# Performance work log

Measured on AMD Instinct MI355X. Metric: run time of the kernel, lower is better.

The kernel has to match this reference:

```python
import jax, jax.numpy as jnp
import numpy as np

B, S, D_IN, D_OUT, H = 4, 2048, 1024, 1024, 16
DH = D_OUT // H


def setup_inputs() -> dict:
    key = jax.random.key(0)
    k1, k2, k3 = jax.random.split(key, 3)
    payload = jax.random.normal(k1, (B, S, D_IN), dtype=jnp.float32)
    w_qkv = jax.random.normal(k2, (D_IN, 3 * D_OUT), dtype=jnp.float32) * (D_IN ** -0.5)
    w_out = jax.random.normal(k3, (D_OUT, D_OUT), dtype=jnp.float32) * (D_OUT ** -0.5)
    b_out = jnp.zeros((D_OUT,), dtype=jnp.float32)
    return {"payload": payload, "w_qkv": w_qkv, "w_out": w_out, "b_out": b_out}


def reference(payload, w_qkv, w_out, b_out):
    b, t, _ = payload.shape
    h, dh = H, DH
    qkv = payload @ w_qkv  # [b, t, 3*D_OUT]
    q, k, v = jnp.split(qkv, 3, axis=-1)
    # [b, t, h, dh] -> [b, h, t, dh]
    q = q.reshape(b, t, h, dh).transpose(0, 2, 1, 3)
    k = k.reshape(b, t, h, dh).transpose(0, 2, 1, 3)
    v = v.reshape(b, t, h, dh).transpose(0, 2, 1, 3)
    scores = jnp.einsum("bhqd,bhkd->bhqk", q, k) / jnp.sqrt(jnp.float32(dh))
    causal = jnp.tril(jnp.ones((t, t), dtype=bool))  # True = keep
    scores = jnp.where(causal, scores, -jnp.inf)
    weights = jax.nn.softmax(scores, axis=-1)
    # dropout_rate = 0.0 -> identity
    ctx = jnp.einsum("bhqk,bhkd->bhqd", weights, v)
    ctx = ctx.transpose(0, 2, 1, 3).reshape(b, t, h * dh)
    return ctx @ w_out + b_out
```

## Files before the change

kernel.cpp:

```cpp
#include <hip/hip_runtime.h>

#define NB 4
#define NS 2048
#define NH 16
#define NDH 64

typedef short bf16x8 __attribute__((ext_vector_type(8)));
typedef short bf16x4 __attribute__((ext_vector_type(4)));
typedef float f32x4 __attribute__((ext_vector_type(4)));
typedef unsigned short u16;
typedef unsigned int u32;

static __device__ __forceinline__ u16 f2bf(float f) {
  unsigned u = __float_as_uint(f);
  u += 0x7fffu + ((u >> 16) & 1u);
  return (u16)(u >> 16);
}

#define GLDS(gp, lp) __builtin_amdgcn_global_load_lds( \
    (const __attribute__((address_space(1))) void*)(gp), \
    (__attribute__((address_space(3))) void*)(lp), 16, 0, 0)

__global__ void prep_k(const float* __restrict__ payload, const float* __restrict__ w_qkv,
                       const float* __restrict__ w_out, u16* __restrict__ Xb,
                       u16* __restrict__ Wqkvt, u16* __restrict__ Woutt) {
  __shared__ float t[32][33];
  const int bid = blockIdx.x;
  if (bid < 4096) {
    int i = (bid * 256 + threadIdx.x) * 8;
    float4 a = *(const float4*)&payload[i];
    float4 b = *(const float4*)&payload[i + 4];
    bf16x8 u;
    u[0] = (short)f2bf(a.x); u[1] = (short)f2bf(a.y);
    u[2] = (short)f2bf(a.z); u[3] = (short)f2bf(a.w);
    u[4] = (short)f2bf(b.x); u[5] = (short)f2bf(b.y);
    u[6] = (short)f2bf(b.z); u[7] = (short)f2bf(b.w);
    *(bf16x8*)&Xb[i] = u;
    return;
  }
  const float* in;  u16* out;  int R, C, c0, r0;
  if (bid < 4096 + 3072) {
    int b2 = bid - 4096;
    in = w_qkv; out = Wqkvt; R = 1024; C = 3072;
    c0 = (b2 % 96) * 32; r0 = (b2 / 96) * 32;
  } else {
    int b3 = bid - 7168;
    in = w_out; out = Woutt; R = 1024; C = 1024;
    c0 = (b3 & 31) * 32; r0 = (b3 >> 5) * 32;
  }
  int tx = threadIdx.x & 7, ty = threadIdx.x >> 3;
  float4 v = *(const float4*)&in[(size_t)(r0 + ty) * C + c0 + tx * 4];
  t[ty][tx * 4 + 0] = v.x; t[ty][tx * 4 + 1] = v.y;
  t[ty][tx * 4 + 2] = v.z; t[ty][tx * 4 + 3] = v.w;
  __syncthreads();
  ushort4 o;
  o.x = f2bf(t[tx * 4 + 0][ty]); o.y = f2bf(t[tx * 4 + 1][ty]);
  o.z = f2bf(t[tx * 4 + 2][ty]); o.w = f2bf(t[tx * 4 + 3][ty]);
  *(ushort4*)&out[(size_t)(c0 + ty) * R + r0 + tx * 4] = o;
}

template<int MODE, int WM>
__global__ __launch_bounds__(WM * 128)
void gemm_k(const u16* __restrict__ A, const u16* __restrict__ Bt,
            int M, int N, int K,
            u16* __restrict__ Qo, u16* __restrict__ Ko, u16* __restrict__ VTo,
            float* __restrict__ Co, const float* __restrict__ bias) {
  constexpr int T  = WM * 128;
  constexpr int BM = WM * 64;
  constexpr int RA = 4;
  constexpr int RB = 1024 / T;
  __shared__ __align__(16) u16 As[BM * 64];
  __shared__ __align__(16) u16 Bs[128 * 64];
  const int tid = threadIdx.x;
  const int w = tid >> 6, l = tid & 63;
  const int lr = l & 15, lg = l >> 4;
  const int wr = w >> 1, wc = w & 1;

  const int L = blockIdx.x + gridDim.x * blockIdx.y;
  const int xcd = L & 7, li = L >> 3;
  const int bx = li % gridDim.x;
  const int by = xcd * (gridDim.y >> 3) + li / gridDim.x;

  const int m0 = by * BM, n0 = bx * 128;
  const int swz = (lr & 7) << 4;

  f32x4 acc[4][4] = {};

  const int nk = K >> 6;
  for (int kt = 0; kt < nk; ++kt) {
    __syncthreads();
    const int k0 = kt * 64;
#pragma unroll
    for (int r2 = 0; r2 < RA; ++r2) {
      int c = r2 * T + tid;
      int row = c >> 3;
      int scolb = ((c & 7) * 16) ^ ((row & 7) << 4);
      GLDS(A + (size_t)(m0 + row) * K + k0 + (scolb >> 1),
           (char*)As + (size_t)r2 * T * 16 + w * 1024);
    }
#pragma unroll
    for (int r2 = 0; r2 < RB; ++r2) {
      int c = r2 * T + tid;
      int row = c >> 3;
      int scolb = ((c & 7) * 16) ^ ((row & 7) << 4);
      GLDS(Bt + (size_t)(n0 + row) * K + k0 + (scolb >> 1),
           (char*)Bs + (size_t)r2 * T * 16 + w * 1024);
    }
    __syncthreads();

#pragma unroll
    for (int kk = 0; kk < 2; ++kk) {
      bf16x8 af[4];
#pragma unroll
      for (int mi = 0; mi < 4; ++mi)
        af[mi] = *(const bf16x8*)((const char*)As +
                  ((wr * 64 + mi * 16 + lr) * 128 + ((kk * 64 + lg * 16) ^ swz)));
#pragma unroll
      for (int ni = 0; ni < 4; ++ni) {
        bf16x8 bfr = *(const bf16x8*)((const char*)Bs +
                  ((wc * 64 + ni * 16 + lr) * 128 + ((kk * 64 + lg * 16) ^ swz)));
#pragma unroll
        for (int mi = 0; mi < 4; ++mi)
          acc[mi][ni] = __builtin_amdgcn_mfma_f32_16x16x32_bf16(af[mi], bfr, acc[mi][ni], 0, 0, 0);
      }
    }
  }

#pragma unroll
  for (int mi = 0; mi < 4; ++mi) {
#pragma unroll
    for (int ni = 0; ni < 4; ++ni) {
#pragma unroll
      for (int r = 0; r < 4; ++r) {
        int gm = m0 + wr * 64 + mi * 16 + lg * 4 + r;
        int gn = n0 + wc * 64 + ni * 16 + lr;
        float v = acc[mi][ni][r];
        if (MODE == 0) {
          int which = gn >> 10, hd = gn & 1023;
          int b = gm >> 11, s = gm & 2047;
          int bh = b * NH + (hd >> 6), dh = hd & 63;
          if (which == 0)      Qo[((size_t)bh * NS + s) * NDH + dh] = f2bf(v * 0.1803368801111204f);
          else if (which == 1) Ko[((size_t)bh * NS + s) * NDH + dh] = f2bf(v);
          else                 VTo[((size_t)bh * NDH + dh) * NS + s] = f2bf(v);
        } else {
          Co[(size_t)gm * N + gn] = v + bias[gn];
        }
      }
    }
  }
}

__global__ __launch_bounds__(512)
void attn_k(const u16* __restrict__ Q, const u16* __restrict__ Kg,
            const u16* __restrict__ VTg, u16* __restrict__ CTX) {
  const int bh = blockIdx.x;
  const int pr = blockIdx.y;
  const int tid = threadIdx.x, w = tid >> 6, l = tid & 63;
  const int lr = l & 15, lg = l >> 4;
  const u16* Qh  = Q   + (size_t)bh * NS * NDH;
  const u16* Kh  = Kg  + (size_t)bh * NS * NDH;
  const u16* Vth = VTg + (size_t)bh * NDH * NS;

  __shared__ __align__(16) u16 Ks[2][128 * 64];
  __shared__ __align__(16) u16 Vs[2][64 * 128];

  const int kRow0 = tid >> 3,         kColb = (tid & 7) * 16;
  const int kRow1 = 64 + (tid >> 3);
  const int vRow0 = tid >> 4,         vColb = (tid & 15) * 16;
  const int vRow1 = 32 + (tid >> 4);
  const int kSrc0 = kRow0 * NDH + ((kColb ^ ((kRow0 & 7) << 4)) >> 1);
  const int kSrc1 = kRow1 * NDH + ((kColb ^ ((kRow1 & 7) << 4)) >> 1);
  const int vSrc0 = vRow0 * NS + ((vColb ^ ((vRow0 & 7) << 4)) >> 1);
  const int vSrc1 = vRow1 * NS + ((vColb ^ ((vRow1 & 7) << 4)) >> 1);
  const int ldsOff0 = w * 1024;
  const int ldsOff1 = 8192 + w * 1024;

#define STAGE(t, buf) do {                                            \
    const u16* Kt_ = Kh  + (size_t)(t) * 128 * NDH;                   \
    const u16* Vt_ = Vth + (size_t)(t) * 128;                         \
    GLDS(Kt_ + kSrc0, (char*)Ks[buf] + ldsOff0);                      \
    GLDS(Kt_ + kSrc1, (char*)Ks[buf] + ldsOff1);                      \
    GLDS(Vt_ + vSrc0, (char*)Vs[buf] + ldsOff0);                      \
    GLDS(Vt_ + vSrc1, (char*)Vs[buf] + ldsOff1);                      \
  } while (0)

  const int swz = (lr & 7) << 4;
  const int b = bh >> 4, h = bh & 15;

  for (int pass = 0; pass < 2; ++pass) {
    const int qt = pass == 0 ? pr : 15 - pr;

    const int qrow = qt * 128 + w * 16 + lr;
    bf16x8 qf[2];
    qf[0] = *(const bf16x8*)&Qh[(size_t)qrow * NDH + 0 * 32 + lg * 8];
    qf[1] = *(const bf16x8*)&Qh[(size_t)qrow * NDH + 1 * 32 + lg * 8];

    f32x4 o[4] = {};
    float lrun = 0.f;
    const int qmin = qt * 128 + w * 16;

    __syncthreads();
    STAGE(0, 0);
    __syncthreads();

    const int NT = qt + 1;
    for (int kt = 0; kt < NT; ++kt) {
      const int cur = kt & 1;
      if (kt + 1 < NT) STAGE(kt + 1, cur ^ 1);

#pragma unroll
      for (int sub = 0; sub < 2; ++sub) {
        f32x4 sc[4] = {};
#pragma unroll
        for (int kk = 0; kk < 2; ++kk) {
#pragma unroll
          for (int kg = 0; kg < 4; ++kg) {
            bf16x8 kf = *(const bf16x8*)((const char*)Ks[cur] +
                         ((sub * 64 + kg * 16 + lr) * 128 + ((kk * 64 + lg * 16) ^ swz)));
            sc[kg] = __builtin_amdgcn_mfma_f32_16x16x32_bf16(kf, qf[kk], sc[kg], 0, 0, 0);
          }
        }

        const int kbase = kt * 128 + sub * 64;
        float sum = 0.f;
        if (kbase + 63 > qmin) {
#pragma unroll
          for (int kg = 0; kg < 4; ++kg)
#pragma unroll
            for (int r = 0; r < 4; ++r) {
              int kglob = kbase + kg * 16 + lg * 4 + r;
              float e = (kglob > qrow) ? 0.f : exp2f(sc[kg][r]);
              sc[kg][r] = e; sum += e;
            }
        } else {
#pragma unroll
          for (int kg = 0; kg < 4; ++kg)
#pragma unroll
            for (int r = 0; r < 4; ++r) {
              float e = exp2f(sc[kg][r]);
              sc[kg][r] = e; sum += e;
            }
        }
        lrun += sum;

#pragma unroll
        for (int half = 0; half < 2; ++half) {
          union { u32 wd[4]; bf16x8 v; } pk;
#pragma unroll
          for (int w2 = 0; w2 < 4; ++w2) {
            float lo = sc[half * 2 + (w2 >> 1)][2 * (w2 & 1)];
            float hi = sc[half * 2 + (w2 >> 1)][2 * (w2 & 1) + 1];
            asm("v_cvt_pk_bf16_f32 %0, %1, %2" : "=v"(pk.wd[w2]) : "v"(lo), "v"(hi));
          }
          bf16x8 pf = pk.v;
#pragma unroll
          for (int dhg = 0; dhg < 4; ++dhg) {
            const char* vrow = (const char*)Vs[cur] + (dhg * 16 + lr) * 256;
            bf16x4 va = *(const bf16x4*)(vrow + sub * 128 + ((half * 64 + lg * 8) ^ swz));
            bf16x4 vb = *(const bf16x4*)(vrow + sub * 128 + ((half * 64 + 32 + lg * 8) ^ swz));
            bf16x8 vf = __builtin_shufflevector(va, vb, 0, 1, 2, 3, 4, 5, 6, 7);
            o[dhg] = __builtin_amdgcn_mfma_f32_16x16x32_bf16(pf, vf, o[dhg], 0, 0, 0);
          }
        }
      }

      __syncthreads();
    }

    lrun += __shfl_xor(lrun, 16);
    lrun += __shfl_xor(lrun, 32);
    float linv = 1.0f / lrun;
#pragma unroll
    for (int r = 0; r < 4; ++r) {
      float lq = __shfl(linv, (l & 48) | (lg * 4 + r));
      int srow = qt * 128 + w * 16 + lg * 4 + r;
      size_t base = ((size_t)(b * NS + srow)) * (NH * NDH) + h * NDH;
#pragma unroll
      for (int dhg = 0; dhg < 4; ++dhg)
        CTX[base + dhg * 16 + lr] = f2bf(o[dhg][r] * lq);
    }
  }
#undef STAGE
}

extern "C" void kernel_launch(void* const* d_in, const int* in_sizes, int n_in,
                              void* d_out, int out_size, void* d_ws, size_t ws_size,
                              hipStream_t stream) {
  const float* payload = (const float*)d_in[0];
  const float* w_qkv   = (const float*)d_in[1];
  const float* w_out   = (const float*)d_in[2];
  const float* b_out   = (const float*)d_in[3];
  float* out = (float*)d_out;

  char* ws = (char*)d_ws;
  size_t o0 = 0;
  u16* Xb    = (u16*)(ws + o0); o0 += (size_t)8192 * 1024 * 2;
  u16* Wqkvt = (u16*)(ws + o0); o0 += (size_t)3072 * 1024 * 2;
  u16* Woutt = (u16*)(ws + o0); o0 += (size_t)1024 * 1024 * 2;
  u16* Qb    = (u16*)(ws + o0); o0 += (size_t)64 * 2048 * 64 * 2;
  u16* Kb    = (u16*)(ws + o0); o0 += (size_t)64 * 2048 * 64 * 2;
  u16* VTb   = (u16*)(ws + o0); o0 += (size_t)64 * 64 * 2048 * 2;
  u16* CTX   = Xb;

  prep_k<<<dim3(8192), dim3(256), 0, stream>>>(payload, w_qkv, w_out, Xb, Wqkvt, Woutt);
  gemm_k<0, 4><<<dim3(24, 32), dim3(512), 0, stream>>>(Xb, Wqkvt, 8192, 3072, 1024,
                                                       Qb, Kb, VTb, nullptr, nullptr);
  attn_k<<<dim3(64, 8), dim3(512), 0, stream>>>(Qb, Kb, VTb, CTX);
  gemm_k<1, 2><<<dim3(8, 64), dim3(256), 0, stream>>>(CTX, Woutt, 8192, 1024, 1024,
                                                      nullptr, nullptr, nullptr, out, b_out);
}
```

Before: 186.2 us.

## Process two 128-row query tiles per warp group to reuse K/V tiles

```diff
diff --git a/kernel.cpp b/kernel.cpp
--- a/kernel.cpp
+++ b/kernel.cpp
@@ -188,78 +188,103 @@
   const int b = bh >> 4, h = bh & 15;
 
   for (int pass = 0; pass < 2; ++pass) {
-    const int qt = pass == 0 ? pr : 15 - pr;
-
-    const int qrow = qt * 128 + w * 16 + lr;
-    bf16x8 qf[2];
-    qf[0] = *(const bf16x8*)&Qh[(size_t)qrow * NDH + 0 * 32 + lg * 8];
-    qf[1] = *(const bf16x8*)&Qh[(size_t)qrow * NDH + 1 * 32 + lg * 8];
-
-    f32x4 o[4] = {};
-    float lrun = 0.f;
-    const int qmin = qt * 128 + w * 16;
+    const int qt = pass == 0 ? pr : 7 - pr;
+
+    const int qrow0 = qt * 256 + w * 16 + lr;
+    const int qrow1 = qrow0 + 128;
+    bf16x8 qf0[2], qf1[2];
+    qf0[0] = *(const bf16x8*)&Qh[(size_t)qrow0 * NDH + 0 * 32 + lg * 8];
+    qf0[1] = *(const bf16x8*)&Qh[(size_t)qrow0 * NDH + 1 * 32 + lg * 8];
+    qf1[0] = *(const bf16x8*)&Qh[(size_t)qrow1 * NDH + 0 * 32 + lg * 8];
+    qf1[1] = *(const bf16x8*)&Qh[(size_t)qrow1 * NDH + 1 * 32 + lg * 8];
+
+    f32x4 o0[4] = {}, o1[4] = {};
+    float lrun0 = 0.f, lrun1 = 0.f;
+    const int qmin0 = qt * 256 + w * 16;
+    const int qmin1 = qmin0 + 128;
 
     __syncthreads();
     STAGE(0, 0);
     __syncthreads();
 
-    const int NT = qt + 1;
+    const int NT = 2 * qt + 2;
     for (int kt = 0; kt < NT; ++kt) {
       const int cur = kt & 1;
       if (kt + 1 < NT) STAGE(kt + 1, cur ^ 1);
 
 #pragma unroll
       for (int sub = 0; sub < 2; ++sub) {
-        f32x4 sc[4] = {};
+        f32x4 sc0[4] = {}, sc1[4] = {};
 #pragma unroll
         for (int kk = 0; kk < 2; ++kk) {
 #pragma unroll
           for (int kg = 0; kg < 4; ++kg) {
             bf16x8 kf = *(const bf16x8*)((const char*)Ks[cur] +
                          ((sub * 64 + kg * 16 + lr) * 128 + ((kk * 64 + lg * 16) ^ swz)));
-            sc[kg] = __builtin_amdgcn_mfma_f32_16x16x32_bf16(kf, qf[kk], sc[kg], 0, 0, 0);
+            sc0[kg] = __builtin_amdgcn_mfma_f32_16x16x32_bf16(kf, qf0[kk], sc0[kg], 0, 0, 0);
+            sc1[kg] = __builtin_amdgcn_mfma_f32_16x16x32_bf16(kf, qf1[kk], sc1[kg], 0, 0, 0);
           }
         }
 
         const int kbase = kt * 128 + sub * 64;
-        float sum = 0.f;
-        if (kbase + 63 > qmin) {
+        float sum0 = 0.f, sum1 = 0.f;
+        if (kbase + 63 > qmin1) {
 #pragma unroll
           for (int kg = 0; kg < 4; ++kg)
 #pragma unroll
             for (int r = 0; r < 4; ++r) {
               int kglob = kbase + kg * 16 + lg * 4 + r;
-              float e = (kglob > qrow) ? 0.f : exp2f(sc[kg][r]);
-              sc[kg][r] = e; sum += e;
+              float e0 = (kglob > qrow0) ? 0.f : exp2f(sc0[kg][r]);
+              float e1 = (kglob > qrow1) ? 0.f : exp2f(sc1[kg][r]);
+              sc0[kg][r] = e0; sum0 += e0;
+              sc1[kg][r] = e1; sum1 += e1;
+            }
+        } else if (kbase + 63 > qmin0) {
+#pragma unroll
+          for (int kg = 0; kg < 4; ++kg)
+#pragma unroll
+            for (int r = 0; r < 4; ++r) {
+              int kglob = kbase + kg * 16 + lg * 4 + r;
+              float e0 = (kglob > qrow0) ? 0.f : exp2f(sc0[kg][r]);
+              float e1 = exp2f(sc1[kg][r]);
+              sc0[kg][r] = e0; sum0 += e0;
+              sc1[kg][r] = e1; sum1 += e1;
             }
         } else {
 #pragma unroll
           for (int kg = 0; kg < 4; ++kg)
 #pragma unroll
             for (int r = 0; r < 4; ++r) {
-              float e = exp2f(sc[kg][r]);
-              sc[kg][r] = e; sum += e;
+              float e0 = exp2f(sc0[kg][r]);
+              float e1 = exp2f(sc1[kg][r]);
+              sc0[kg][r] = e0; sum0 += e0;
+              sc1[kg][r] = e1; sum1 += e1;
             }
         }
-        lrun += sum;
+        lrun0 += sum0;
+        lrun1 += sum1;
 
 #pragma unroll
         for (int half = 0; half < 2; ++half) {
-          union { u32 wd[4]; bf16x8 v; } pk;
+          union { u32 wd[4]; bf16x8 v; } pk0, pk1;
 #pragma unroll
           for (int w2 = 0; w2 < 4; ++w2) {
-            float lo = sc[half * 2 + (w2 >> 1)][2 * (w2 & 1)];
-            float hi = sc[half * 2 + (w2 >> 1)][2 * (w2 & 1) + 1];
-            asm("v_cvt_pk_bf16_f32 %0, %1, %2" : "=v"(pk.wd[w2]) : "v"(lo), "v"(hi));
+            float lo0 = sc0[half * 2 + (w2 >> 1)][2 * (w2 & 1)];
+            float hi0 = sc0[half * 2 + (w2 >> 1)][2 * (w2 & 1) + 1];
+            asm("v_cvt_pk_bf16_f32 %0, %1, %2" : "=v"(pk0.wd[w2]) : "v"(lo0), "v"(hi0));
+            float lo1 = sc1[half * 2 + (w2 >> 1)][2 * (w2 & 1)];
+            float hi1 = sc1[half * 2 + (w2 >> 1)][2 * (w2 & 1) + 1];
+            asm("v_cvt_pk_bf16_f32 %0, %1, %2" : "=v"(pk1.wd[w2]) : "v"(lo1), "v"(hi1));
           }
-          bf16x8 pf = pk.v;
+          bf16x8 pf0 = pk0.v, pf1 = pk1.v;
 #pragma unroll
           for (int dhg = 0; dhg < 4; ++dhg) {
             const char* vrow = (const char*)Vs[cur] + (dhg * 16 + lr) * 256;
             bf16x4 va = *(const bf16x4*)(vrow + sub * 128 + ((half * 64 + lg * 8) ^ swz));
             bf16x4 vb = *(const bf16x4*)(vrow + sub * 128 + ((half * 64 + 32 + lg * 8) ^ swz));
             bf16x8 vf = __builtin_shufflevector(va, vb, 0, 1, 2, 3, 4, 5, 6, 7);
-            o[dhg] = __builtin_amdgcn_mfma_f32_16x16x32_bf16(pf, vf, o[dhg], 0, 0, 0);
+            o0[dhg] = __builtin_amdgcn_mfma_f32_16x16x32_bf16(pf0, vf, o0[dhg], 0, 0, 0);
+            o1[dhg] = __builtin_amdgcn_mfma_f32_16x16x32_bf16(pf1, vf, o1[dhg], 0, 0, 0);
           }
         }
       }
@@ -267,17 +292,21 @@
       __syncthreads();
     }
 
-    lrun += __shfl_xor(lrun, 16);
-    lrun += __shfl_xor(lrun, 32);
-    float linv = 1.0f / lrun;
+    lrun0 += __shfl_xor(lrun0, 16); lrun0 += __shfl_xor(lrun0, 32);
+    lrun1 += __shfl_xor(lrun1, 16); lrun1 += __shfl_xor(lrun1, 32);
+    float linv0 = 1.0f / lrun0, linv1 = 1.0f / lrun1;
 #pragma unroll
     for (int r = 0; r < 4; ++r) {
-      float lq = __shfl(linv, (l & 48) | (lg * 4 + r));
-      int srow = qt * 128 + w * 16 + lg * 4 + r;
-      size_t base = ((size_t)(b * NS + srow)) * (NH * NDH) + h * NDH;
-#pragma unroll
-      for (int dhg = 0; dhg < 4; ++dhg)
-        CTX[base + dhg * 16 + lr] = f2bf(o[dhg][r] * lq);
+      float lq0 = __shfl(linv0, (l & 48) | (lg * 4 + r));
+      float lq1 = __shfl(linv1, (l & 48) | (lg * 4 + r));
+      int srow = qt * 256 + w * 16 + lg * 4 + r;
+      size_t base0 = ((size_t)(b * NS + srow)) * (NH * NDH) + h * NDH;
+      size_t base1 = ((size_t)(b * NS + srow + 128)) * (NH * NDH) + h * NDH;
+#pragma unroll
+      for (int dhg = 0; dhg < 4; ++dhg) {
+        CTX[base0 + dhg * 16 + lr] = f2bf(o0[dhg][r] * lq0);
+        CTX[base1 + dhg * 16 + lr] = f2bf(o1[dhg][r] * lq1);
+      }
     }
   }
 #undef STAGE
@@ -305,7 +334,7 @@
   prep_k<<<dim3(8192), dim3(256), 0, stream>>>(payload, w_qkv, w_out, Xb, Wqkvt, Woutt);
   gemm_k<0, 4><<<dim3(24, 32), dim3(512), 0, stream>>>(Xb, Wqkvt, 8192, 3072, 1024,
                                                        Qb, Kb, VTb, nullptr, nullptr);
-  attn_k<<<dim3(64, 8), dim3(512), 0, stream>>>(Qb, Kb, VTb, CTX);
+  attn_k<<<dim3(64, 4), dim3(512), 0, stream>>>(Qb, Kb, VTb, CTX);
   gemm_k<1, 2><<<dim3(8, 64), dim3(256), 0, stream>>>(CTX, Woutt, 8192, 1024, 1024,
                                                       nullptr, nullptr, nullptr, out, b_out);
 }
```

Result: no change. 189.7 us (+1.9%).

## Add double-buffered pipelined QKV projection GEMM with split-phase LDS staging

Applied to the files above, without the earlier changes.

```diff
diff --git a/kernel.cpp b/kernel.cpp
--- a/kernel.cpp
+++ b/kernel.cpp
@@ -20,6 +20,12 @@
 #define GLDS(gp, lp) __builtin_amdgcn_global_load_lds( \
     (const __attribute__((address_space(1))) void*)(gp), \
     (__attribute__((address_space(3))) void*)(lp), 16, 0, 0)
+
+#define BAR do { __builtin_amdgcn_sched_barrier(0); \
+                 __builtin_amdgcn_s_barrier(); \
+                 __builtin_amdgcn_sched_barrier(0); } while (0)
+#define VMC0 do { asm volatile("s_waitcnt vmcnt(0)" ::: "memory"); \
+                  __builtin_amdgcn_sched_barrier(0); } while (0)
 
 __global__ void prep_k(const float* __restrict__ payload, const float* __restrict__ w_qkv,
                        const float* __restrict__ w_out, u16* __restrict__ Xb,
@@ -59,11 +65,120 @@
   *(ushort4*)&out[(size_t)(c0 + ty) * R + r0 + tx * 4] = o;
 }
 
-template<int MODE, int WM>
+__global__ __launch_bounds__(512)
+void gemm0p_k(const u16* __restrict__ A, const u16* __restrict__ Bt,
+              u16* __restrict__ Qo, u16* __restrict__ Ko, u16* __restrict__ VTo) {
+  constexpr int K = 1024, NKT = 16;
+  __shared__ __align__(16) u16 As[2][256 * 64];
+  __shared__ __align__(16) u16 Bs[2][128 * 64];
+  const int tid = threadIdx.x, w = tid >> 6, l = tid & 63;
+  const int lr = l & 15, lg = l >> 4;
+  const int wr = w >> 1, wc = w & 1;
+
+  const int L = blockIdx.x + gridDim.x * blockIdx.y;
+  const int xcd = L & 7, li = L >> 3;
+  const int bx = li % gridDim.x;
+  const int by = xcd * (gridDim.y >> 3) + li / gridDim.x;
+  const int m0 = by * 256, n0 = bx * 128;
+  const int swz = (lr & 7) << 4;
+
+  int src[4], dst[4];
+#pragma unroll
+  for (int r2 = 0; r2 < 4; ++r2) {
+    int c = r2 * 512 + tid;
+    int row = c >> 3;
+    int scolb = ((c & 7) * 16) ^ ((row & 7) << 4);
+    src[r2] = row * K + (scolb >> 1);
+    dst[r2] = r2 * 8192 + w * 1024;
+  }
+
+#define STG_A(t, buf) do {                                         \
+    const u16* Ab_ = A + (size_t)m0 * K + (t) * 64;                \
+    GLDS(Ab_ + src[0], (char*)As[buf] + dst[0]);                   \
+    GLDS(Ab_ + src[1], (char*)As[buf] + dst[1]);                   \
+    GLDS(Ab_ + src[2], (char*)As[buf] + dst[2]);                   \
+    GLDS(Ab_ + src[3], (char*)As[buf] + dst[3]);                   \
+  } while (0)
+#define STG_B(t, buf) do {                                         \
+    const u16* Bb_ = Bt + (size_t)n0 * K + (t) * 64;               \
+    GLDS(Bb_ + src[0], (char*)Bs[buf] + dst[0]);                   \
+    GLDS(Bb_ + src[1], (char*)Bs[buf] + dst[1]);                   \
+  } while (0)
+
+  f32x4 acc[4][4] = {};
+
+  STG_A(0, 0); STG_B(0, 0);
+  VMC0;
+  BAR;
+
+  for (int t = 0; t < NKT; ++t) {
+    const int cur = t & 1, nxt = cur ^ 1;
+    const char* Ar = (const char*)As[cur];
+    const char* Br = (const char*)Bs[cur];
+
+    bf16x8 af[4], bfr[4];
+#pragma unroll
+    for (int mi = 0; mi < 4; ++mi)
+      af[mi] = *(const bf16x8*)(Ar + (wr * 64 + mi * 16 + lr) * 128 + ((lg * 16) ^ swz));
+#pragma unroll
+    for (int ni = 0; ni < 4; ++ni)
+      bfr[ni] = *(const bf16x8*)(Br + (wc * 64 + ni * 16 + lr) * 128 + ((lg * 16) ^ swz));
+    if (t + 1 < NKT) STG_A(t + 1, nxt);
+    BAR;
+    __builtin_amdgcn_s_setprio(1);
+#pragma unroll
+    for (int ni = 0; ni < 4; ++ni)
+#pragma unroll
+      for (int mi = 0; mi < 4; ++mi)
+        acc[mi][ni] = __builtin_amdgcn_mfma_f32_16x16x32_bf16(af[mi], bfr[ni], acc[mi][ni], 0, 0, 0);
+    __builtin_amdgcn_s_setprio(0);
+    BAR;
+
+#pragma unroll
+    for (int mi = 0; mi < 4; ++mi)
+      af[mi] = *(const bf16x8*)(Ar + (wr * 64 + mi * 16 + lr) * 128 + ((64 + lg * 16) ^ swz));
+#pragma unroll
+    for (int ni = 0; ni < 4; ++ni)
+      bfr[ni] = *(const bf16x8*)(Br + (wc * 64 + ni * 16 + lr) * 128 + ((64 + lg * 16) ^ swz));
+    if (t + 1 < NKT) STG_B(t + 1, nxt);
+    BAR;
+    __builtin_amdgcn_s_setprio(1);
+#pragma unroll
+    for (int ni = 0; ni < 4; ++ni)
+#pragma unroll
+      for (int mi = 0; mi < 4; ++mi)
+        acc[mi][ni] = __builtin_amdgcn_mfma_f32_16x16x32_bf16(af[mi], bfr[ni], acc[mi][ni], 0, 0, 0);
+    __builtin_amdgcn_s_setprio(0);
+    VMC0;
+    BAR;
+  }
+
+#pragma unroll
+  for (int mi = 0; mi < 4; ++mi) {
+#pragma unroll
+    for (int ni = 0; ni < 4; ++ni) {
+#pragma unroll
+      for (int r = 0; r < 4; ++r) {
+        int gm = m0 + wr * 64 + mi * 16 + lg * 4 + r;
+        int gn = n0 + wc * 64 + ni * 16 + lr;
+        float v = acc[mi][ni][r];
+        int which = gn >> 10, hd = gn & 1023;
+        int b = gm >> 11, s = gm & 2047;
+        int bh = b * NH + (hd >> 6), dh = hd & 63;
+        if (which == 0)      Qo[((size_t)bh * NS + s) * NDH + dh] = f2bf(v * 0.1803368801111204f);
+        else if (which == 1) Ko[((size_t)bh * NS + s) * NDH + dh] = f2bf(v);
+        else                 VTo[((size_t)bh * NDH + dh) * NS + s] = f2bf(v);
+      }
+    }
+  }
+#undef STG_A
+#undef STG_B
+}
+
+template<int WM>
 __global__ __launch_bounds__(WM * 128)
 void gemm_k(const u16* __restrict__ A, const u16* __restrict__ Bt,
             int M, int N, int K,
-            u16* __restrict__ Qo, u16* __restrict__ Ko, u16* __restrict__ VTo,
             float* __restrict__ Co, const float* __restrict__ bias) {
   constexpr int T  = WM * 128;
   constexpr int BM = WM * 64;
@@ -127,27 +242,15 @@
   }
 
 #pragma unroll
-  for (int mi = 0; mi < 4; ++mi) {
-#pragma unroll
-    for (int ni = 0; ni < 4; ++ni) {
+  for (int mi = 0; mi < 4; ++mi)
+#pragma unroll
+    for (int ni = 0; ni < 4; ++ni)
 #pragma unroll
       for (int r = 0; r < 4; ++r) {
         int gm = m0 + wr * 64 + mi * 16 + lg * 4 + r;
         int gn = n0 + wc * 64 + ni * 16 + lr;
-        float v = acc[mi][ni][r];
-        if (MODE == 0) {
-          int which = gn >> 10, hd = gn & 1023;
-          int b = gm >> 11, s = gm & 2047;
-          int bh = b * NH + (hd >> 6), dh = hd & 63;
-          if (which == 0)      Qo[((size_t)bh * NS + s) * NDH + dh] = f2bf(v * 0.1803368801111204f);
-          else if (which == 1) Ko[((size_t)bh * NS + s) * NDH + dh] = f2bf(v);
-          else                 VTo[((size_t)bh * NDH + dh) * NS + s] = f2bf(v);
-        } else {
-          Co[(size_t)gm * N + gn] = v + bias[gn];
-        }
+        Co[(size_t)gm * N + gn] = acc[mi][ni][r] + bias[gn];
       }
-    }
-  }
 }
 
 __global__ __launch_bounds__(512)
@@ -303,9 +406,8 @@
   u16* CTX   = Xb;
 
   prep_k<<<dim3(8192), dim3(256), 0, stream>>>(payload, w_qkv, w_out, Xb, Wqkvt, Woutt);
-  gemm_k<0, 4><<<dim3(24, 32), dim3(512), 0, stream>>>(Xb, Wqkvt, 8192, 3072, 1024,
-                                                       Qb, Kb, VTb, nullptr, nullptr);
+  gemm0p_k<<<dim3(24, 32), dim3(512), 0, stream>>>(Xb, Wqkvt, Qb, Kb, VTb);
   attn_k<<<dim3(64, 8), dim3(512), 0, stream>>>(Qb, Kb, VTb, CTX);
-  gemm_k<1, 2><<<dim3(8, 64), dim3(256), 0, stream>>>(CTX, Woutt, 8192, 1024, 1024,
-                                                      nullptr, nullptr, nullptr, out, b_out);
-}
+  gemm_k<2><<<dim3(8, 64), dim3(256), 0, stream>>>(CTX, Woutt, 8192, 1024, 1024,
+                                                   out, b_out);
+}
```

Result: no change. 189.7 us (+1.9%).
